# Optimization experiments

Measured on AMD Instinct MI355X. Metric: run time of the kernel, lower is better.

## Reference

```python
import jax, jax.numpy as jnp
import numpy as np

BATCH, SEQ, IN_DIM, HID, OUT = 256, 256, 128, 1024, 10

def setup_inputs() -> dict:
    key = jax.random.key(0)
    k = jax.random.split(key, 6)
    s = lambda d: 1.0 / np.sqrt(d)
    return {
        "x":   jax.random.normal(k[0], (BATCH, SEQ, IN_DIM), dtype=jnp.float32),
        "Whx": jax.random.normal(k[1], (IN_DIM, HID), dtype=jnp.float32) * s(IN_DIM),
        "Whh": jax.random.normal(k[2], (HID, HID), dtype=jnp.float32) * s(HID),
        "bh":  jax.random.normal(k[3], (HID,), dtype=jnp.float32) * 0.01,
        "Why": jax.random.normal(k[4], (HID, OUT), dtype=jnp.float32) * s(HID),
        "bo":  jax.random.normal(k[5], (OUT,), dtype=jnp.float32) * 0.01,
    }

def reference(x, Whx, Whh, bh, Why, bo):
    # Precompute input projections for all timesteps in one big GEMM:
    # [B,S,I] @ [I,H] -> [B,S,H]
    xproj = jnp.einsum("bsi,ih->bsh", x, Whx) + bh
    # Sequential tanh recurrence; h0 = 0 reproduces the t==0 branch
    # (tanh(x0@Whx + bh) == tanh(x0@Whx + 0@Whh + bh)).
    h0 = jnp.zeros((x.shape[0], Whh.shape[0]), dtype=x.dtype)

    def step(h, xp_t):
        h = jnp.tanh(xp_t + h @ Whh)
        return h, None

    h_final, _ = jax.lax.scan(step, h0, jnp.swapaxes(xproj, 0, 1))  # scan over seq
    o = h_final @ Why + bo
    return jax.nn.softmax(o, axis=1)
```

## Files before the change

kernel.cpp:

```cpp
#include <hip/hip_runtime.h>
#include <hip/hip_bf16.h>

#define BATCH 256
#define SEQ   256
#define IND   128
#define HID   1024
#define OUTD  10

#define NCOLG 16
#define NROWG 16
#define ROWG_ELEMS (HID*16)
#define CTR_OFF (2*BATCH*HID)

typedef __bf16 bf16x8 __attribute__((ext_vector_type(8)));
typedef float  f32x4  __attribute__((ext_vector_type(4)));
typedef unsigned long long u64;

union Pack4 { u64 q; __bf16 h[4]; };
union Pack8 { u64 q[2]; bf16x8 v; };

__device__ __forceinline__ float fast_tanh(float z) {
    float e = __expf(-2.0f * fabsf(z));
    float t = (1.0f - e) / (1.0f + e);
    return copysignf(t, z);
}

__global__ __launch_bounds__(256, 1)
void rnn_persistent(const float* __restrict__ x,
                    const float* __restrict__ Whx,
                    const float* __restrict__ Whh,
                    const float* __restrict__ bh,
                    const float* __restrict__ Why,
                    const float* __restrict__ bo,
                    float* __restrict__ out,
                    __bf16* __restrict__ ws)
{
    const int tid  = threadIdx.x;
    const int lane = tid & 63;
    const int wave = tid >> 6;
    const int bx   = blockIdx.x;
    const int colg = bx & (NCOLG-1);
    const int rowg = bx >> 4;
    const int c0 = colg * 64;
    const int r0 = rowg * 16;
    const int ln15 = lane & 15;
    const int quad = lane >> 4;

    __bf16* hb = ws;
    int* flags  = (int*)(ws + CTR_OFF);
    int* myflag = flags + rowg*16 + colg;
    int* pollp  = flags + rowg*16 + wave*4 + (lane & 3);

    __shared__ float red[4][16][64];

    bf16x8 whh_hi[4][8];
    #pragma unroll
    for (int ct = 0; ct < 4; ++ct) {
        const int nn = c0 + ct*16 + ln15;
        #pragma unroll
        for (int c = 0; c < 8; ++c) {
            const int kb = wave*256 + c*32 + quad*8;
            #pragma unroll
            for (int j = 0; j < 8; ++j)
                whh_hi[ct][c][j] = (__bf16)Whh[(size_t)(kb + j)*HID + nn];
        }
    }
    bf16x8 whx_hi[4], whx_lo[4];
    #pragma unroll
    for (int ct = 0; ct < 4; ++ct) {
        const int nn = c0 + ct*16 + ln15;
        const int kb = wave*32 + quad*8;
        #pragma unroll
        for (int j = 0; j < 8; ++j) {
            float v = Whx[(size_t)(kb + j)*HID + nn];
            __bf16 h = (__bf16)v;
            whx_hi[ct][j] = h;
            whx_lo[ct][j] = (__bf16)(v - (float)h);
        }
    }
    const int srow = tid >> 4;
    const int scol = (tid & 15) * 4;
    const float4 bh4 = *(const float4*)(bh + c0 + scol);
    const size_t xrow_base = (size_t)(r0 + ln15) * (SEQ*IND) + wave*32 + quad*8;
    const int sc = c0 + scol;
    const int soffq = (sc >> 5)*128 + (((sc & 31) >> 3)*16 + srow)*2 + ((sc >> 2) & 1);

    for (int t = 0; t < SEQ; ++t) {
        const int cur = t & 1;
        const int nxt = cur ^ 1;
        f32x4 acc0{}, acc1{}, acc2{}, acc3{};

        {
            const float* xp = x + xrow_base + (size_t)t*IND;
            float4 v0 = ((const float4*)xp)[0];
            float4 v1 = ((const float4*)xp)[1];
            float vv[8] = {v0.x,v0.y,v0.z,v0.w,v1.x,v1.y,v1.z,v1.w};
            bf16x8 ahi, alo;
            #pragma unroll
            for (int j = 0; j < 8; ++j) {
                __bf16 h = (__bf16)vv[j];
                ahi[j] = h;
                alo[j] = (__bf16)(vv[j] - (float)h);
            }
            acc0 = __builtin_amdgcn_mfma_f32_16x16x32_bf16(ahi, whx_hi[0], acc0, 0,0,0);
            acc0 = __builtin_amdgcn_mfma_f32_16x16x32_bf16(alo, whx_hi[0], acc0, 0,0,0);
            acc0 = __builtin_amdgcn_mfma_f32_16x16x32_bf16(ahi, whx_lo[0], acc0, 0,0,0);
            acc1 = __builtin_amdgcn_mfma_f32_16x16x32_bf16(ahi, whx_hi[1], acc1, 0,0,0);
            acc1 = __builtin_amdgcn_mfma_f32_16x16x32_bf16(alo, whx_hi[1], acc1, 0,0,0);
            acc1 = __builtin_amdgcn_mfma_f32_16x16x32_bf16(ahi, whx_lo[1], acc1, 0,0,0);
            acc2 = __builtin_amdgcn_mfma_f32_16x16x32_bf16(ahi, whx_hi[2], acc2, 0,0,0);
            acc2 = __builtin_amdgcn_mfma_f32_16x16x32_bf16(alo, whx_hi[2], acc2, 0,0,0);
            acc2 = __builtin_amdgcn_mfma_f32_16x16x32_bf16(ahi, whx_lo[2], acc2, 0,0,0);
            acc3 = __builtin_amdgcn_mfma_f32_16x16x32_bf16(ahi, whx_hi[3], acc3, 0,0,0);
            acc3 = __builtin_amdgcn_mfma_f32_16x16x32_bf16(alo, whx_hi[3], acc3, 0,0,0);
            acc3 = __builtin_amdgcn_mfma_f32_16x16x32_bf16(ahi, whx_lo[3], acc3, 0,0,0);
        }

        if (t > 0) {
            for (;;) {
                int v = __hip_atomic_load(pollp, __ATOMIC_RELAXED, __HIP_MEMORY_SCOPE_AGENT);
                if (__all(v >= t)) break;
            }
            asm volatile("" ::: "memory");

            const u64* hq = (const u64*)(hb + (size_t)(cur*NROWG + rowg)*ROWG_ELEMS);
            Pack8 pa[8];
            #pragma unroll
            for (int c = 0; c < 8; ++c) {
                const int idx = (wave*8 + c)*128 + lane*2;
                pa[c].q[0] = __hip_atomic_load(hq + idx,     __ATOMIC_RELAXED, __HIP_MEMORY_SCOPE_AGENT);
                pa[c].q[1] = __hip_atomic_load(hq + idx + 1, __ATOMIC_RELAXED, __HIP_MEMORY_SCOPE_AGENT);
            }
            __builtin_amdgcn_sched_group_barrier(0x020, 16, 0);
            __builtin_amdgcn_sched_group_barrier(0x008, 32, 0);
            #pragma unroll
            for (int c = 0; c < 8; ++c) {
                acc0 = __builtin_amdgcn_mfma_f32_16x16x32_bf16(pa[c].v, whh_hi[0][c], acc0, 0,0,0);
                acc1 = __builtin_amdgcn_mfma_f32_16x16x32_bf16(pa[c].v, whh_hi[1][c], acc1, 0,0,0);
                acc2 = __builtin_amdgcn_mfma_f32_16x16x32_bf16(pa[c].v, whh_hi[2][c], acc2, 0,0,0);
                acc3 = __builtin_amdgcn_mfma_f32_16x16x32_bf16(pa[c].v, whh_hi[3][c], acc3, 0,0,0);
            }
        }

        #pragma unroll
        for (int r = 0; r < 4; ++r) {
            const int row = quad*4 + r;
            red[wave][row][ln15]      = acc0[r];
            red[wave][row][16 + ln15] = acc1[r];
            red[wave][row][32 + ln15] = acc2[r];
            red[wave][row][48 + ln15] = acc3[r];
        }
        __syncthreads();
        {
            const float4 s0 = *(const float4*)&red[0][srow][scol];
            const float4 s1 = *(const float4*)&red[1][srow][scol];
            const float4 s2 = *(const float4*)&red[2][srow][scol];
            const float4 s3 = *(const float4*)&red[3][srow][scol];
            float z0 = s0.x + s1.x + s2.x + s3.x + bh4.x;
            float z1 = s0.y + s1.y + s2.y + s3.y + bh4.y;
            float z2 = s0.z + s1.z + s2.z + s3.z + bh4.z;
            float z3 = s0.w + s1.w + s2.w + s3.w + bh4.w;
            Pack4 pk;
            pk.h[0] = (__bf16)fast_tanh(z0);
            pk.h[1] = (__bf16)fast_tanh(z1);
            pk.h[2] = (__bf16)fast_tanh(z2);
            pk.h[3] = (__bf16)fast_tanh(z3);
            u64* hnq = (u64*)(hb + (size_t)(nxt*NROWG + rowg)*ROWG_ELEMS) + soffq;
            __hip_atomic_store(hnq, pk.q, __ATOMIC_RELAXED, __HIP_MEMORY_SCOPE_AGENT);
        }
        __syncthreads();
        if (tid == 0) {
            __hip_atomic_store(myflag, t + 1, __ATOMIC_RELAXED, __HIP_MEMORY_SCOPE_AGENT);
        }
    }

    if (colg == 0) {
        int* epip = flags + rowg*16 + (lane & 15);
        for (;;) {
            int v = __hip_atomic_load(epip, __ATOMIC_RELAXED, __HIP_MEMORY_SCOPE_AGENT);
            if (__all(v >= SEQ)) break;
        }
        asm volatile("" ::: "memory");
        __syncthreads();
        const u64* hq0 = (const u64*)(hb + (size_t)(0*NROWG + rowg)*ROWG_ELEMS);
        float* obuf = &red[0][0][0];
        for (int idx = tid; idx < 16*OUTD; idx += 256) {
            const int row = idx / OUTD;
            const int c   = idx - row*OUTD;
            float s = bo[c];
            #pragma unroll 8
            for (int k4 = 0; k4 < HID/4; ++k4) {
                const int k = k4*4;
                Pack4 p;
                p.q = __hip_atomic_load(hq0 + (k>>5)*128 + (((k&31)>>3)*16 + row)*2 + ((k>>2)&1),
                                        __ATOMIC_RELAXED, __HIP_MEMORY_SCOPE_AGENT);
                const float* wr = Why + (size_t)k*OUTD + c;
                s += (float)p.h[0]*wr[0] + (float)p.h[1]*wr[OUTD]
                   + (float)p.h[2]*wr[2*OUTD] + (float)p.h[3]*wr[3*OUTD];
            }
            obuf[idx] = s;
        }
        __syncthreads();
        if (tid < 16) {
            float m = -1e30f;
            #pragma unroll
            for (int c = 0; c < OUTD; ++c) m = fmaxf(m, obuf[tid*OUTD+c]);
            float e[OUTD]; float ssum = 0.f;
            #pragma unroll
            for (int c = 0; c < OUTD; ++c) { e[c] = __expf(obuf[tid*OUTD+c] - m); ssum += e[c]; }
            const float inv = 1.0f / ssum;
            #pragma unroll
            for (int c = 0; c < OUTD; ++c) out[(size_t)(r0+tid)*OUTD + c] = e[c]*inv;
        }
    }
}

extern "C" void kernel_launch(void* const* d_in, const int* in_sizes, int n_in,
                              void* d_out, int out_size, void* d_ws, size_t ws_size,
                              hipStream_t stream)
{
    const float* x   = (const float*)d_in[0];
    const float* Whx = (const float*)d_in[1];
    const float* Whh = (const float*)d_in[2];
    const float* bh  = (const float*)d_in[3];
    const float* Why = (const float*)d_in[4];
    const float* bo  = (const float*)d_in[5];
    float* out = (float*)d_out;
    __bf16* ws = (__bf16*)d_ws;

    hipMemsetAsync((char*)d_ws + (size_t)CTR_OFF*sizeof(__bf16), 0,
                   (size_t)2048, stream);

    void* args[] = { &x, &Whx, &Whh, &bh, &Why, &bo, &out, &ws };
    hipLaunchCooperativeKernel((const void*)rnn_persistent,
                               dim3(NROWG*NCOLG), dim3(256), args, 0, stream);
}
```

Measured before the change: 865.6 us.

## Use per-wave 16-bit flags and double-buffered LDS to drop trailing barrier

Replaces the per-block int step flag with one 16-bit flag per wave, published by lane 0 after an s_waitcnt on that wave's own h stores, so the second __syncthreads per timestep is removed. Consumers now poll 16 per-wave flags per row group instead of 4 per-block flags. The LDS reduction buffer is double-buffered by step parity, with padding to 68 columns to reduce bank conflicts, so a fast wave writing the next step's partials cannot clobber data still being read. This shortens the per-step critical path of the sequential recurrence but adds polling traffic and relies on relaxed atomics plus vmcnt waits for ordering.

```diff
diff --git a/kernel.cpp b/kernel.cpp
--- a/kernel.cpp
+++ b/kernel.cpp
@@ -15,6 +15,7 @@
 typedef __bf16 bf16x8 __attribute__((ext_vector_type(8)));
 typedef float  f32x4  __attribute__((ext_vector_type(4)));
 typedef unsigned long long u64;
+typedef unsigned short ushort_t;
 
 union Pack4 { u64 q; __bf16 h[4]; };
 union Pack8 { u64 q[2]; bf16x8 v; };
@@ -24,6 +25,7 @@
     float t = (1.0f - e) / (1.0f + e);
     return copysignf(t, z);
 }
+
 
 __global__ __launch_bounds__(256, 1)
 void rnn_persistent(const float* __restrict__ x,
@@ -47,11 +49,11 @@
     const int quad = lane >> 4;
 
     __bf16* hb = ws;
-    int* flags  = (int*)(ws + CTR_OFF);
-    int* myflag = flags + rowg*16 + colg;
-    int* pollp  = flags + rowg*16 + wave*4 + (lane & 3);
-
-    __shared__ float red[4][16][64];
+    ushort_t* wflags = (ushort_t*)(ws + CTR_OFF);
+    ushort_t* myflag = wflags + (rowg*64 + colg*4 + wave);
+    ushort_t* pollp  = wflags + (rowg*64 + wave*16 + ln15);
+
+    __shared__ float red[2][4][16][68];
 
     bf16x8 whh_hi[4][8];
     #pragma unroll
@@ -118,8 +120,8 @@
 
         if (t > 0) {
             for (;;) {
-                int v = __hip_atomic_load(pollp, __ATOMIC_RELAXED, __HIP_MEMORY_SCOPE_AGENT);
-                if (__all(v >= t)) break;
+                ushort_t v = __hip_atomic_load(pollp, __ATOMIC_RELAXED, __HIP_MEMORY_SCOPE_AGENT);
+                if (__all((int)v >= t)) break;
             }
             asm volatile("" ::: "memory");
 
@@ -145,17 +147,17 @@
         #pragma unroll
         for (int r = 0; r < 4; ++r) {
             const int row = quad*4 + r;
-            red[wave][row][ln15]      = acc0[r];
-            red[wave][row][16 + ln15] = acc1[r];
-            red[wave][row][32 + ln15] = acc2[r];
-            red[wave][row][48 + ln15] = acc3[r];
+            red[cur][wave][row][ln15]      = acc0[r];
+            red[cur][wave][row][16 + ln15] = acc1[r];
+            red[cur][wave][row][32 + ln15] = acc2[r];
+            red[cur][wave][row][48 + ln15] = acc3[r];
         }
         __syncthreads();
         {
-            const float4 s0 = *(const float4*)&red[0][srow][scol];
-            const float4 s1 = *(const float4*)&red[1][srow][scol];
-            const float4 s2 = *(const float4*)&red[2][srow][scol];
-            const float4 s3 = *(const float4*)&red[3][srow][scol];
+            const float4 s0 = *(const float4*)&red[cur][0][srow][scol];
+            const float4 s1 = *(const float4*)&red[cur][1][srow][scol];
+            const float4 s2 = *(const float4*)&red[cur][2][srow][scol];
+            const float4 s3 = *(const float4*)&red[cur][3][srow][scol];
             float z0 = s0.x + s1.x + s2.x + s3.x + bh4.x;
             float z1 = s0.y + s1.y + s2.y + s3.y + bh4.y;
             float z2 = s0.z + s1.z + s2.z + s3.z + bh4.z;
@@ -168,22 +170,22 @@
             u64* hnq = (u64*)(hb + (size_t)(nxt*NROWG + rowg)*ROWG_ELEMS) + soffq;
             __hip_atomic_store(hnq, pk.q, __ATOMIC_RELAXED, __HIP_MEMORY_SCOPE_AGENT);
         }
-        __syncthreads();
-        if (tid == 0) {
-            __hip_atomic_store(myflag, t + 1, __ATOMIC_RELAXED, __HIP_MEMORY_SCOPE_AGENT);
+        asm volatile("s_waitcnt vmcnt(0)" ::: "memory");
+        if (lane == 0) {
+            __hip_atomic_store(myflag, (ushort_t)(t + 1), __ATOMIC_RELAXED, __HIP_MEMORY_SCOPE_AGENT);
         }
     }
 
     if (colg == 0) {
-        int* epip = flags + rowg*16 + (lane & 15);
+        ushort_t* epip = wflags + rowg*64 + lane;
         for (;;) {
-            int v = __hip_atomic_load(epip, __ATOMIC_RELAXED, __HIP_MEMORY_SCOPE_AGENT);
-            if (__all(v >= SEQ)) break;
+            ushort_t v = __hip_atomic_load(epip, __ATOMIC_RELAXED, __HIP_MEMORY_SCOPE_AGENT);
+            if (__all((int)v >= SEQ)) break;
         }
         asm volatile("" ::: "memory");
         __syncthreads();
         const u64* hq0 = (const u64*)(hb + (size_t)(0*NROWG + rowg)*ROWG_ELEMS);
-        float* obuf = &red[0][0][0];
+        float* obuf = &red[0][0][0][0];
         for (int idx = tid; idx < 16*OUTD; idx += 256) {
             const int row = idx / OUTD;
             const int c   = idx - row*OUTD;
```

New measurement: 1.131 ms. +30.7%, slower.

## Embed parity tags in hidden-state bf16 words to replace flag polling

Applied to the files above, without the earlier changes.

Each step writes a parity tag into the exponent MSB of two bf16 hidden values per 64-bit store. Because tanh outputs stay below 2, that bit is otherwise always zero. Consumers issue the hidden-state loads early, overlapping them with the input-projection MFMAs, then validate the tags and reload until they match. This removes the separate flag-poll-then-load round trip on each step. The flag poll remains as a fallback after several retries, and the tag bits are masked off before use. The memset now clears the whole hidden buffer, which adds launch-time work.

```diff
diff --git a/kernel.cpp b/kernel.cpp
--- a/kernel.cpp
+++ b/kernel.cpp
@@ -16,7 +16,9 @@
 typedef float  f32x4  __attribute__((ext_vector_type(4)));
 typedef unsigned long long u64;
 
-union Pack4 { u64 q; __bf16 h[4]; };
+#define TAGMASK ((1ULL<<14) | (1ULL<<46))
+
+union Pack4 { u64 q; __bf16 h[4]; unsigned short u[4]; };
 union Pack8 { u64 q[2]; bf16x8 v; };
 
 __device__ __forceinline__ float fast_tanh(float z) {
@@ -24,6 +26,7 @@
     float t = (1.0f - e) / (1.0f + e);
     return copysignf(t, z);
 }
+
 
 __global__ __launch_bounds__(256, 1)
 void rnn_persistent(const float* __restrict__ x,
@@ -90,6 +93,17 @@
         const int nxt = cur ^ 1;
         f32x4 acc0{}, acc1{}, acc2{}, acc3{};
 
+        Pack8 pa[8];
+        const u64* hq = (const u64*)(hb + (size_t)(cur*NROWG + rowg)*ROWG_ELEMS);
+        if (t > 0) {
+            #pragma unroll
+            for (int c = 0; c < 8; ++c) {
+                const int idx = (wave*8 + c)*128 + lane*2;
+                pa[c].q[0] = __hip_atomic_load(hq + idx,     __ATOMIC_RELAXED, __HIP_MEMORY_SCOPE_AGENT);
+                pa[c].q[1] = __hip_atomic_load(hq + idx + 1, __ATOMIC_RELAXED, __HIP_MEMORY_SCOPE_AGENT);
+            }
+        }
+
         {
             const float* xp = x + xrow_base + (size_t)t*IND;
             float4 v0 = ((const float4*)xp)[0];
@@ -117,21 +131,44 @@
         }
 
         if (t > 0) {
-            for (;;) {
-                int v = __hip_atomic_load(pollp, __ATOMIC_RELAXED, __HIP_MEMORY_SCOPE_AGENT);
-                if (__all(v >= t)) break;
-            }
-            asm volatile("" ::: "memory");
-
-            const u64* hq = (const u64*)(hb + (size_t)(cur*NROWG + rowg)*ROWG_ELEMS);
-            Pack8 pa[8];
+            const u64 want = (u64)((((unsigned)t + 1u) >> 1) & 1u);
+            bool good = false;
+            #pragma unroll 1
+            for (int r = 0; r < 8; ++r) {
+                unsigned ok = 1u;
+                #pragma unroll
+                for (int c = 0; c < 8; ++c) {
+                    ok &= (unsigned)(((pa[c].q[0] >> 14) & 1ULL) == want);
+                    ok &= (unsigned)(((pa[c].q[0] >> 46) & 1ULL) == want);
+                    ok &= (unsigned)(((pa[c].q[1] >> 14) & 1ULL) == want);
+                    ok &= (unsigned)(((pa[c].q[1] >> 46) & 1ULL) == want);
+                }
+                if (__all((int)ok)) { good = true; break; }
+                #pragma unroll
+                for (int c = 0; c < 8; ++c) {
+                    const int idx = (wave*8 + c)*128 + lane*2;
+                    pa[c].q[0] = __hip_atomic_load(hq + idx,     __ATOMIC_RELAXED, __HIP_MEMORY_SCOPE_AGENT);
+                    pa[c].q[1] = __hip_atomic_load(hq + idx + 1, __ATOMIC_RELAXED, __HIP_MEMORY_SCOPE_AGENT);
+                }
+            }
+            if (!good) {
+                for (;;) {
+                    int v = __hip_atomic_load(pollp, __ATOMIC_RELAXED, __HIP_MEMORY_SCOPE_AGENT);
+                    if (__all(v >= t)) break;
+                }
+                asm volatile("" ::: "memory");
+                #pragma unroll
+                for (int c = 0; c < 8; ++c) {
+                    const int idx = (wave*8 + c)*128 + lane*2;
+                    pa[c].q[0] = __hip_atomic_load(hq + idx,     __ATOMIC_RELAXED, __HIP_MEMORY_SCOPE_AGENT);
+                    pa[c].q[1] = __hip_atomic_load(hq + idx + 1, __ATOMIC_RELAXED, __HIP_MEMORY_SCOPE_AGENT);
+                }
+            }
             #pragma unroll
             for (int c = 0; c < 8; ++c) {
-                const int idx = (wave*8 + c)*128 + lane*2;
-                pa[c].q[0] = __hip_atomic_load(hq + idx,     __ATOMIC_RELAXED, __HIP_MEMORY_SCOPE_AGENT);
-                pa[c].q[1] = __hip_atomic_load(hq + idx + 1, __ATOMIC_RELAXED, __HIP_MEMORY_SCOPE_AGENT);
-            }
-            __builtin_amdgcn_sched_group_barrier(0x020, 16, 0);
+                pa[c].q[0] &= ~TAGMASK;
+                pa[c].q[1] &= ~TAGMASK;
+            }
             __builtin_amdgcn_sched_group_barrier(0x008, 32, 0);
             #pragma unroll
             for (int c = 0; c < 8; ++c) {
@@ -165,6 +202,9 @@
             pk.h[1] = (__bf16)fast_tanh(z1);
             pk.h[2] = (__bf16)fast_tanh(z2);
             pk.h[3] = (__bf16)fast_tanh(z3);
+            const unsigned ntag = (((unsigned)t + 2u) >> 1) & 1u;
+            pk.u[0] = (unsigned short)(pk.u[0] | (ntag << 14));
+            pk.u[2] = (unsigned short)(pk.u[2] | (ntag << 14));
             u64* hnq = (u64*)(hb + (size_t)(nxt*NROWG + rowg)*ROWG_ELEMS) + soffq;
             __hip_atomic_store(hnq, pk.q, __ATOMIC_RELAXED, __HIP_MEMORY_SCOPE_AGENT);
         }
@@ -194,6 +234,7 @@
                 Pack4 p;
                 p.q = __hip_atomic_load(hq0 + (k>>5)*128 + (((k&31)>>3)*16 + row)*2 + ((k>>2)&1),
                                         __ATOMIC_RELAXED, __HIP_MEMORY_SCOPE_AGENT);
+                p.q &= ~TAGMASK;
                 const float* wr = Why + (size_t)k*OUTD + c;
                 s += (float)p.h[0]*wr[0] + (float)p.h[1]*wr[OUTD]
                    + (float)p.h[2]*wr[2*OUTD] + (float)p.h[3]*wr[3*OUTD];
@@ -228,8 +269,7 @@
     float* out = (float*)d_out;
     __bf16* ws = (__bf16*)d_ws;
 
-    hipMemsetAsync((char*)d_ws + (size_t)CTR_OFF*sizeof(__bf16), 0,
-                   (size_t)2048, stream);
+    hipMemsetAsync(d_ws, 0, (size_t)CTR_OFF*sizeof(__bf16) + 2048, stream);
 
     void* args[] = { &x, &Whx, &Whh, &bh, &Why, &bo, &out, &ws };
     hipLaunchCooperativeKernel((const void*)rnn_persistent,
```

Measured after the change: 1.087 ms. +25.6%, slower.
